# Kernel optimization log

Hardware: AMD Instinct MI355X
Metric: run time of the kernel (lower is better)

## Reference

```python
import jax, jax.numpy as jnp
import numpy as np
from jax import lax

B, C, H, W = 2, 64, 384, 384
WS = 8; NH = 4; HD = C // NH; S = WS * WS  # 64 tokens per window
EPS = 1e-5


def setup_inputs() -> dict:
    key = jax.random.key(0)
    ks = jax.random.split(key, 16)
    def n(k, shape, s=0.02):
        return jax.random.normal(k, shape, jnp.float32) * s
    return {
        "x": jax.random.normal(ks[0], (B, C, H, W), jnp.float32),
        "norm1_w": jnp.ones((C,), jnp.float32), "norm1_b": jnp.zeros((C,), jnp.float32),
        "qkv_w": n(ks[1], (3 * C, C)), "qkv_b": jnp.zeros((3 * C,), jnp.float32),
        "pos_bias": n(ks[2], (1, S, NH, NH), 0.01),  # faithful: bias over (tokens, heads, heads)
        "out_w": n(ks[3], (C, C)), "out_b": jnp.zeros((C,), jnp.float32),
        "convp_w": n(ks[4], (C, C)), "convp_b": jnp.zeros((C,), jnp.float32),
        "pw1_w": n(ks[5], (C, C, 1)), "pw1_b": jnp.zeros((C,), jnp.float32),
        "dw1_w": n(ks[6], (C, 1, 3)), "dw1_b": jnp.zeros((C,), jnp.float32),
        "tok_w": n(ks[7], (C, C)), "tok_b": jnp.zeros((C,), jnp.float32),
        "norm2_w": jnp.ones((C,), jnp.float32), "norm2_b": jnp.zeros((C,), jnp.float32),
        "leff_pw_w": n(ks[8], (C, C, 1, 1)),
        "leff_dw_w": n(ks[9], (C, 1, 3, 3)), "leff_dw_b": jnp.zeros((C,), jnp.float32),
        "fc1_w": n(ks[10], (4 * C, C)), "fc1_b": jnp.zeros((4 * C,), jnp.float32),
        "fc2_w": n(ks[11], (C, 4 * C)), "fc2_b": jnp.zeros((C,), jnp.float32),
    }


def _ln_c(x, w, b):
    # channel-wise LayerNorm (Restormer 'WithBias') on (B,C,H,W), biased variance
    mu = x.mean(axis=1, keepdims=True)
    var = ((x - mu) ** 2).mean(axis=1, keepdims=True)
    return (x - mu) / jnp.sqrt(var + EPS) * w[None, :, None, None] + b[None, :, None, None]


def _lin(x, w, b):
    return x @ w.T + b


def _win_part(x):
    # (B,C,H,W) -> (B*nw, S, C); H,W divisible by WS so pad is a no-op
    b = x.shape[0]
    x = x.reshape(b, C, H // WS, WS, W // WS, WS)
    return x.transpose(0, 2, 4, 3, 5, 1).reshape(-1, S, C)


def _win_merge(wins):
    b = wins.shape[0] // ((H // WS) * (W // WS))
    x = wins.reshape(b, H // WS, W // WS, WS, WS, C)
    return x.transpose(0, 5, 1, 3, 2, 4).reshape(b, C, H, W)


def _remsa(xw, qkv_w, qkv_b, pos_bias, out_w, out_b, convp_w, convp_b,
           pw1_w, pw1_b, dw1_w, dw1_b, tok_w, tok_b):
    bw = xw.shape[0]
    qkv = _lin(xw, qkv_w, qkv_b).reshape(bw, S, NH, 3 * HD)
    q, k, v = jnp.split(qkv, 3, axis=-1)  # each (bw, S, NH, HD)
    # Faithful to source: NO head transpose -> attention mixes across the heads axis
    scores = jnp.einsum('bshd,bsgd->bshg', q, k) * (HD ** -0.5) + pos_bias  # (bw,S,NH,NH)
    attn = jax.nn.softmax(scores, axis=-1)
    ao = jnp.einsum('bshg,bsgd->bshd', attn, v).reshape(bw, S, C)
    ao = _lin(ao, out_w, out_b)
    # convolutional branch
    xc = _lin(xw, convp_w, convp_b).transpose(0, 2, 1)  # (bw, C, S)
    xc = jnp.einsum('bcs,oc->bos', xc, pw1_w[:, :, 0]) + pw1_b[None, :, None]  # 1x1 conv1d
    xc = lax.conv_general_dilated(xc, dw1_w, (1,), 'SAME', feature_group_count=C,
                                  dimension_numbers=('NCH', 'OIH', 'NCH')) + dw1_b[None, :, None]
    xc = _lin(xc.transpose(0, 2, 1), tok_w, tok_b)
    return ao + xc


def _leff(x, pw_w, dw_w, dw_b, fc1_w, fc1_b, fc2_w, fc2_b):
    b = x.shape[0]
    y = lax.conv_general_dilated(x, pw_w, (1, 1), 'SAME',
                                 dimension_numbers=('NCHW', 'OIHW', 'NCHW'))  # 1x1, no bias
    y = lax.conv_general_dilated(y, dw_w, (1, 1), 'SAME', feature_group_count=C,
                                 dimension_numbers=('NCHW', 'OIHW', 'NCHW')) + dw_b[None, :, None, None]
    y = y.transpose(0, 2, 3, 1).reshape(b, H * W, C)
    y = jax.nn.gelu(_lin(y, fc1_w, fc1_b), approximate=False)
    y = _lin(y, fc2_w, fc2_b)
    return y.reshape(b, H, W, C).transpose(0, 3, 1, 2)


def reference(x, norm1_w, norm1_b, qkv_w, qkv_b, pos_bias, out_w, out_b,
              convp_w, convp_b, pw1_w, pw1_b, dw1_w, dw1_b, tok_w, tok_b,
              norm2_w, norm2_b, leff_pw_w, leff_dw_w, leff_dw_b,
              fc1_w, fc1_b, fc2_w, fc2_b):
    xw = _win_part(_ln_c(x, norm1_w, norm1_b))
    r = _win_merge(_remsa(xw, qkv_w, qkv_b, pos_bias, out_w, out_b, convp_w, convp_b,
                          pw1_w, pw1_b, dw1_w, dw1_b, tok_w, tok_b))
    x = x + r
    x = x + _leff(_ln_c(x, norm2_w, norm2_b), leff_pw_w, leff_dw_w, leff_dw_b,
                  fc1_w, fc1_b, fc2_w, fc2_b)
    return x
```

## Files before the change

### kernel.cpp

```cpp
#include <hip/hip_runtime.h>
#include <hip/hip_bf16.h>
#include <math.h>

#define Bn 2
#define Cc 64
#define Hh 384
#define Ww 384
#define HW (Hh*Ww)
#define Tt (Bn*HW)

using f32x4  = __attribute__((ext_vector_type(4))) float;
using bf16x8 = __attribute__((ext_vector_type(8))) short;


__device__ __forceinline__ unsigned short f2bf_u(float f) {
  return __builtin_bit_cast(unsigned short, __float2bfloat16(f));
}
__device__ __forceinline__ float bf2f(unsigned short u) {
  union { unsigned u; float f; } v; v.u = ((unsigned)u) << 16;
  return v.f;
}
__device__ __forceinline__ float gelu_exact(float v) {
  return 0.5f * v * (1.0f + erff(v * 0.70710678118654752f));
}


__global__ __launch_bounds__(512, 4) void kA(
    const float* __restrict__ x, unsigned short* __restrict__ x1g, unsigned short* __restrict__ yg,
    const float* __restrict__ n1w, const float* __restrict__ n1b,
    const float* __restrict__ qkvw, const float* __restrict__ qkvb,
    const float* __restrict__ posb,
    const float* __restrict__ outw, const float* __restrict__ outb,
    const float* __restrict__ cpw, const float* __restrict__ cpb,
    const float* __restrict__ pw1w, const float* __restrict__ pw1b,
    const float* __restrict__ dw1w, const float* __restrict__ dw1b,
    const float* __restrict__ tokw, const float* __restrict__ tokb,
    const float* __restrict__ n2w, const float* __restrict__ n2b,
    const float* __restrict__ lpw) {
  __shared__ char sX[16384];
  __shared__ char sW0[8192];
  __shared__ char sW1[8192];
  __shared__ char sQ[49152];

  const int tid = threadIdx.x;
  const int lane = tid & 63, wid = tid >> 6;
  const int fr = lane & 15, kq = lane >> 4;
  const int rtok = wid * 16 + fr;
  const int c0own = kq * 16;
  const int iy = wid, ix = fr;
  const int blk = blockIdx.x;
  const int b = blk / 1152;
  const int rr = blk - b * 1152;
  const int wy = rr / 24, wxp = rr - (rr / 24) * 24;
  const int h0 = wy * 8, w0 = wxp * 16;
  const long ibase = (long)b * HW;

  float4 wr0, wr1;
  const int wrow = tid >> 3, wc0 = (tid & 7) * 8;
  auto WLOAD = [&](const float* g) {
    const float* p = g + (long)wrow * 64 + wc0;
    wr0 = *(const float4*)p; wr1 = *(const float4*)(p + 4);
  };
  auto WSTORE = [&](char* dst) {
    bf16x8 o;
    o[0]=(short)f2bf_u(wr0.x); o[1]=(short)f2bf_u(wr0.y); o[2]=(short)f2bf_u(wr0.z); o[3]=(short)f2bf_u(wr0.w);
    o[4]=(short)f2bf_u(wr1.x); o[5]=(short)f2bf_u(wr1.y); o[6]=(short)f2bf_u(wr1.z); o[7]=(short)f2bf_u(wr1.w);
    *(bf16x8*)(dst + wrow * 128 + ((2 * wc0) ^ ((wrow & 7) << 4))) = o;
  };

  WLOAD(cpw);
  const float* xb = x + ((long)(b * 64 + c0own)) * HW + (long)(h0 + iy) * Ww + (w0 + ix);
  float vx[16]; float s0 = 0.f, s1 = 0.f;
#pragma unroll
  for (int k = 0; k < 16; ++k) {
    float v = xb[(long)k * HW];
    vx[k] = v; s0 += v; s1 += v * v;
  }
  s0 += __shfl_xor(s0, 16); s0 += __shfl_xor(s0, 32);
  s1 += __shfl_xor(s1, 16); s1 += __shfl_xor(s1, 32);
  {
    float m = s0 * (1.f / 64.f);
    float ri = rsqrtf(s1 * (1.f / 64.f) - m * m + 1e-5f);
    const int swz = (rtok & 7) << 4;
#pragma unroll
    for (int q8 = 0; q8 < 2; ++q8) {
      bf16x8 o;
#pragma unroll
      for (int j = 0; j < 8; ++j) {
        int c = c0own + q8 * 8 + j;
        o[j] = (short)f2bf_u((vx[q8 * 8 + j] - m) * ri * n1w[c] + n1b[c]);
      }
      *(bf16x8*)(sX + rtok * 128 + ((c0own * 2 + q8 * 16) ^ swz)) = o;
    }
  }
  WSTORE(sW0); WLOAD(pw1w);
  __syncthreads();

  f32x4 acc[4], res[4];
  auto ZERO = [&](f32x4 a[4]) {
#pragma unroll
    for (int nt = 0; nt < 4; ++nt) a[nt] = (f32x4){0.f, 0.f, 0.f, 0.f};
  };
  auto GEMM = [&](const char* A, const char* W, f32x4 a[4]) {
    __builtin_amdgcn_s_setprio(1);
#pragma unroll
    for (int kh = 0; kh < 2; ++kh) {
      const int arow = wid * 16 + fr;
      bf16x8 af = *(const bf16x8*)(A + arow * 128 + ((kh * 64 + kq * 16) ^ ((arow & 7) << 4)));
#pragma unroll
      for (int nt = 0; nt < 4; ++nt) {
        const int brow = nt * 16 + fr;
        bf16x8 bv = *(const bf16x8*)(W + brow * 128 + ((kh * 64 + kq * 16) ^ ((brow & 7) << 4)));
        a[nt] = __builtin_amdgcn_mfma_f32_16x16x32_bf16(af, bv, a[nt], 0, 0, 0);
      }
    }
    __builtin_amdgcn_s_setprio(0);
  };
  auto EPI = [&](char* dst, f32x4 a[4], const float* bias) {
    const int rb = wid * 16 + kq * 4;
#pragma unroll
    for (int nt = 0; nt < 4; ++nt) {
      const int col = nt * 16 + fr;
      const float bv = bias[col];
#pragma unroll
      for (int reg = 0; reg < 4; ++reg) {
        const int row = rb + reg;
        *(unsigned short*)(dst + row * 128 + ((2 * col) ^ ((row & 7) << 4))) = f2bf_u(a[nt][reg] + bv);
      }
    }
  };
  char* t0 = sQ; char* t1 = sQ + 16384; char* t2 = sQ + 32768;
  float* sQf = (float*)sQ;

  ZERO(acc); GEMM(sX, sW0, acc); EPI(t0, acc, cpb);
  WSTORE(sW1); WLOAD(tokw);
  __syncthreads();
  ZERO(acc); GEMM(t0, sW1, acc); EPI(t1, acc, pw1b);
  WSTORE(sW0); WLOAD(qkvw);
  __syncthreads();
  {
    const int c = tid & 63, tq = tid >> 6;
    const int wl = tq >> 2, chunk = tq & 3;
    float wv0 = dw1w[c * 3], wv1 = dw1w[c * 3 + 1], wv2 = dw1w[c * 3 + 2], bia = dw1b[c];
#pragma unroll
    for (int k = 0; k < 16; ++k) {
      int s = chunk * 16 + k;
      int r0 = ((s >> 3) << 4) + wl * 8 + (s & 7);
      float v = bia + bf2f(*(const unsigned short*)(t1 + r0 * 128 + ((2 * c) ^ ((r0 & 7) << 4)))) * wv1;
      if (s > 0) {
        int rm = (((s - 1) >> 3) << 4) + wl * 8 + ((s - 1) & 7);
        v += bf2f(*(const unsigned short*)(t1 + rm * 128 + ((2 * c) ^ ((rm & 7) << 4)))) * wv0;
      }
      if (s < 63) {
        int rp = (((s + 1) >> 3) << 4) + wl * 8 + ((s + 1) & 7);
        v += bf2f(*(const unsigned short*)(t1 + rp * 128 + ((2 * c) ^ ((rp & 7) << 4)))) * wv2;
      }
      *(unsigned short*)(t0 + r0 * 128 + ((2 * c) ^ ((r0 & 7) << 4))) = f2bf_u(v);
    }
  }
  WSTORE(sW1); WLOAD(qkvw + 4096);
  __syncthreads();
  ZERO(res); GEMM(t0, sW0, res);
  __syncthreads();
  ZERO(acc); GEMM(sX, sW1, acc); EPI(t0, acc, qkvb);
  WSTORE(sW0); WLOAD(qkvw + 8192);
  __syncthreads();
  ZERO(acc); GEMM(sX, sW0, acc); EPI(t1, acc, qkvb + 64);
  WSTORE(sW1); WLOAD(outw);
  __syncthreads();
  ZERO(acc); GEMM(sX, sW1, acc); EPI(t2, acc, qkvb + 128);
  WSTORE(sW0); WLOAD(lpw);
  __syncthreads();
  {
    const int r = rtok;
    const int h = kq;
    const int s = ((r >> 4) << 3) + (r & 7);
    const int swz = (r & 7) << 4;
    auto LD16 = [&](int gcol, float* o) {
      const char* base = sQ + ((gcol >> 6) * 16384) + r * 128;
      int c0 = (gcol & 63) * 2;
      bf16x8 u = *(const bf16x8*)(base + (c0 ^ swz));
      bf16x8 w2_ = *(const bf16x8*)(base + ((c0 + 16) ^ swz));
#pragma unroll
      for (int j = 0; j < 8; ++j) {
        o[j] = bf2f((unsigned short)u[j]); o[8 + j] = bf2f((unsigned short)w2_[j]);
      }
    };
    float q0[16];
    LD16(48 * h, q0);
    float sc[4];
#pragma unroll
    for (int g = 0; g < 4; ++g) {
      float kk[16]; LD16(48 * g + 16, kk);
      float a = 0.f;
#pragma unroll
      for (int d = 0; d < 16; ++d) a += q0[d] * kk[d];
      sc[g] = a * 0.25f + posb[s * 16 + h * 4 + g];
    }
    float m = fmaxf(fmaxf(sc[0], sc[1]), fmaxf(sc[2], sc[3]));
    float e[4]; float tsum = 0.f;
#pragma unroll
    for (int g = 0; g < 4; ++g) { e[g] = __expf(sc[g] - m); tsum += e[g]; }
    float inv = 1.f / tsum;
    float ao[16];
#pragma unroll
    for (int d = 0; d < 16; ++d) ao[d] = 0.f;
#pragma unroll
    for (int g = 0; g < 4; ++g) {
      float vv[16]; LD16(48 * g + 32, vv);
#pragma unroll
      for (int d = 0; d < 16; ++d) ao[d] += e[g] * vv[d];
    }
    bf16x8 o1, o2;
#pragma unroll
    for (int j = 0; j < 8; ++j) { o1[j] = (short)f2bf_u(ao[j] * inv); o2[j] = (short)f2bf_u(ao[8 + j] * inv); }
    *(bf16x8*)(sX + r * 128 + ((h * 32) ^ swz)) = o1;
    *(bf16x8*)(sX + r * 128 + ((h * 32 + 16) ^ swz)) = o2;
  }
  WSTORE(sW1);
  __syncthreads();
  GEMM(sX, sW0, res);
  {
    const int rb = wid * 16 + kq * 4;
#pragma unroll
    for (int nt = 0; nt < 4; ++nt) {
      const int col = nt * 16 + fr;
      const float ob = outb[col] + tokb[col];
#pragma unroll
      for (int reg = 0; reg < 4; ++reg)
        sQf[(rb + reg) * 67 + col] = res[nt][reg] + ob;
    }
  }
  {
    float ss0 = 0.f, ss1 = 0.f;
#pragma unroll
    for (int k = 0; k < 16; ++k) {
      float v = sQf[rtok * 67 + c0own + k] + vx[k];
      vx[k] = v; ss0 += v; ss1 += v * v;
    }
    ss0 += __shfl_xor(ss0, 16); ss0 += __shfl_xor(ss0, 32);
    ss1 += __shfl_xor(ss1, 16); ss1 += __shfl_xor(ss1, 32);
    float m = ss0 * (1.f / 64.f);
    float ri = rsqrtf(ss1 * (1.f / 64.f) - m * m + 1e-5f);
    const int swz = (rtok & 7) << 4;
    long t = ibase + (long)(h0 + iy) * Ww + (w0 + ix);
#pragma unroll
    for (int q8 = 0; q8 < 2; ++q8) {
      bf16x8 xo, no;
#pragma unroll
      for (int j = 0; j < 8; ++j) {
        int c = c0own + q8 * 8 + j;
        float v = vx[q8 * 8 + j];
        xo[j] = (short)f2bf_u(v);
        no[j] = (short)f2bf_u((v - m) * ri * n2w[c] + n2b[c]);
      }
      *(bf16x8*)((char*)x1g + t * 128 + (c0own + q8 * 8) * 2) = xo;
      *(bf16x8*)(sX + rtok * 128 + ((c0own * 2 + q8 * 16) ^ swz)) = no;
    }
  }
  ZERO(acc); GEMM(sX, sW1, acc);
  {
    const int rb = wid * 16 + kq * 4;
#pragma unroll
    for (int nt = 0; nt < 4; ++nt) {
      const int col = nt * 16 + fr;
#pragma unroll
      for (int reg = 0; reg < 4; ++reg)
        sQf[(rb + reg) * 67 + col] = acc[nt][reg];
    }
  }
  {
    long t = ibase + (long)(h0 + iy) * Ww + (w0 + ix);
#pragma unroll
    for (int q8 = 0; q8 < 2; ++q8) {
      bf16x8 o;
#pragma unroll
      for (int j = 0; j < 8; ++j)
        o[j] = (short)f2bf_u(sQf[rtok * 67 + c0own + q8 * 8 + j]);
      *(bf16x8*)((char*)yg + t * 128 + (c0own + q8 * 8) * 2) = o;
    }
  }
}


__global__ __launch_bounds__(512, 2) void kB(
    const unsigned short* __restrict__ yg, const unsigned short* __restrict__ x1g,
    float* __restrict__ out,
    const float* __restrict__ ldw, const float* __restrict__ ldb,
    const float* __restrict__ f1w, const float* __restrict__ f1b,
    const float* __restrict__ f2w, const float* __restrict__ f2b) {
  __shared__ char sZ0[8192];
  __shared__ char sZ1[8192];
  __shared__ char U[33792];
  __shared__ float wtab[640];

  const int tid = threadIdx.x;
  const int lane = tid & 63, wid = tid >> 6;
  const int fr = lane & 15, kq = lane >> 4;
  const int t_own = wid >> 2;
  const int wv = wid & 3;
  const int bid = blockIdx.x;
  const int b = bid / 1152;
  const int r2 = bid - b * 1152;
  const int hp = r2 / 6, wseg = r2 - (r2 / 6) * 6;
  const int h0 = hp * 2, w0 = wseg * 64;
  const long ibase = (long)b * HW;
  const int cbase = fr;
  const int rbase = wv * 16 + kq * 4;

  float4 wr0, wr1;
  const int wrow = tid >> 3, wc0 = (tid & 7) * 8;
  auto WLOAD = [&](const float* g, int rs) {
    const float* p = g + (long)wrow * rs + wc0;
    wr0 = *(const float4*)p; wr1 = *(const float4*)(p + 4);
  };
  auto WSTORE = [&](char* dst) {
    bf16x8 o;
    o[0]=(short)f2bf_u(wr0.x); o[1]=(short)f2bf_u(wr0.y); o[2]=(short)f2bf_u(wr0.z); o[3]=(short)f2bf_u(wr0.w);
    o[4]=(short)f2bf_u(wr1.x); o[5]=(short)f2bf_u(wr1.y); o[6]=(short)f2bf_u(wr1.z); o[7]=(short)f2bf_u(wr1.w);
    *(bf16x8*)(dst + wrow * 128 + ((2 * wc0) ^ ((wrow & 7) << 4))) = o;
  };

  unsigned short x1r[4][4];
  {
    const long p0t = ibase + (long)(h0 + t_own) * Ww + w0;
#pragma unroll
    for (int nt = 0; nt < 4; ++nt) {
      int col = nt * 16 + cbase;
#pragma unroll
      for (int reg = 0; reg < 4; ++reg)
        x1r[nt][reg] = x1g[(p0t + rbase + reg) * 64 + col];
    }
  }

#pragma unroll
  for (int it = 0; it < 2; ++it) {
    int idx = it * 512 + tid;
    if (idx < 576) wtab[idx] = ldw[(idx & 63) * 9 + (idx >> 6)];
    else if (idx < 640) wtab[idx] = ldb[idx - 576];
  }

  for (int it = 0; it < 5; ++it) {
    int idx = it * 512 + tid;
    if (idx >= 2112) break;
    int hr = idx / 528;
    int rq = idx - hr * 528;
    int px = rq >> 3, c8 = rq & 7;
    int h = h0 - 1 + hr, w = w0 - 1 + px;
    uint4 v = make_uint4(0, 0, 0, 0);
    if (h >= 0 && h < Hh && w >= 0 && w < Ww) {
      long t = ibase + (long)h * Ww + w;
      v = *(const uint4*)((const char*)yg + t * 128 + c8 * 16);
    }
    int X = hr * 66 + px;
    *(uint4*)(U + X * 128 + ((c8 * 16) ^ ((X & 7) << 4))) = v;
  }
  WLOAD(f1w, 64);
  __syncthreads();

  {
    const int c8l = tid & 7;
    const int c0 = c8l * 8;
#pragma unroll
    for (int it = 0; it < 2; ++it) {
      int task = it * 512 + tid;
      int r = task >> 9;
      int px = (task >> 3) & 63;
      float a8[8];
#pragma unroll
      for (int j = 0; j < 8; ++j) a8[j] = wtab[576 + c0 + j];
#pragma unroll
      for (int dy = 0; dy < 3; ++dy)
#pragma unroll
        for (int dx = 0; dx < 3; ++dx) {
          int X = (r + dy) * 66 + px + dx;
          bf16x8 v = *(const bf16x8*)(U + X * 128 + ((c8l * 16) ^ ((X & 7) << 4)));
          const float* wk = wtab + (dy * 3 + dx) * 64 + c0;
#pragma unroll
          for (int j = 0; j < 8; ++j) a8[j] += bf2f((unsigned short)v[j]) * wk[j];
        }
      char* sZ = r ? sZ1 : sZ0;
      bf16x8 o;
#pragma unroll
      for (int j = 0; j < 8; ++j) o[j] = (short)f2bf_u(a8[j]);
      *(bf16x8*)(sZ + px * 128 + ((c8l * 16) ^ ((px & 7) << 4))) = o;
    }
  }
  __syncthreads();

  char* sWa = U;
  char* sH0 = U + 8192;
  char* sH1 = U + 16384;
  char* sWb = U + 24576;
  char* sZt = t_own ? sZ1 : sZ0;
  char* sHt = t_own ? sH1 : sH0;
  f32x4 res[4];
#pragma unroll
  for (int nt = 0; nt < 4; ++nt) res[nt] = (f32x4){0.f, 0.f, 0.f, 0.f};

  WSTORE(sWa);
  WLOAD(f2w, 256);
  __syncthreads();

  for (int jc = 0; jc < 4; ++jc) {
    {
      f32x4 acc[4];
#pragma unroll
      for (int nt = 0; nt < 4; ++nt) acc[nt] = (f32x4){0.f, 0.f, 0.f, 0.f};
      __builtin_amdgcn_s_setprio(1);
#pragma unroll
      for (int kh = 0; kh < 2; ++kh) {
        const int arow = wv * 16 + fr;
        bf16x8 af = *(const bf16x8*)(sZt + arow * 128 + ((kh * 64 + kq * 16) ^ ((arow & 7) << 4)));
#pragma unroll
        for (int nt = 0; nt < 4; ++nt) {
          const int brow = nt * 16 + fr;
          bf16x8 bv = *(const bf16x8*)(sWa + brow * 128 + ((kh * 64 + kq * 16) ^ ((brow & 7) << 4)));
          acc[nt] = __builtin_amdgcn_mfma_f32_16x16x32_bf16(af, bv, acc[nt], 0, 0, 0);
        }
      }
      __builtin_amdgcn_s_setprio(0);
      WSTORE(sWb);
      if (jc < 3) WLOAD(f1w + (jc + 1) * 4096, 64);
#pragma unroll
      for (int nt = 0; nt < 4; ++nt) {
        const int col = nt * 16 + cbase;
        const float bv = f1b[jc * 64 + col];
#pragma unroll
        for (int reg = 0; reg < 4; ++reg) {
          const int row = rbase + reg;
          *(unsigned short*)(sHt + row * 128 + ((col * 2) ^ ((row & 7) << 4))) =
              f2bf_u(gelu_exact(acc[nt][reg] + bv));
        }
      }
    }
    __syncthreads();
    __builtin_amdgcn_s_setprio(1);
#pragma unroll
    for (int kh = 0; kh < 2; ++kh) {
      const int arow = wv * 16 + fr;
      bf16x8 af = *(const bf16x8*)(sHt + arow * 128 + ((kh * 64 + kq * 16) ^ ((arow & 7) << 4)));
#pragma unroll
      for (int nt = 0; nt < 4; ++nt) {
        const int brow = nt * 16 + fr;
        bf16x8 bv = *(const bf16x8*)(sWb + brow * 128 + ((kh * 64 + kq * 16) ^ ((brow & 7) << 4)));
        res[nt] = __builtin_amdgcn_mfma_f32_16x16x32_bf16(af, bv, res[nt], 0, 0, 0);
      }
    }
    __builtin_amdgcn_s_setprio(0);
    if (jc < 3) { WSTORE(sWa); WLOAD(f2w + (jc + 1) * 64, 256); }
    __syncthreads();
  }

  float* sO = (float*)U;
#pragma unroll
  for (int nt = 0; nt < 4; ++nt) {
    const int col = nt * 16 + cbase;
    const float bv = f2b[col];
#pragma unroll
    for (int reg = 0; reg < 4; ++reg) {
      const int row = rbase + reg;
      sO[t_own * 4160 + row * 65 + col] = res[nt][reg] + bv + bf2f(x1r[nt][reg]);
    }
  }
  __syncthreads();
  {
    const int t = tid >> 8;
    const int tt = tid & 255;
#pragma unroll
    for (int it = 0; it < 16; ++it) {
      int c = it * 4 + (tt >> 6);
      int wo = tt & 63;
      out[(((long)(b * Cc + c)) * Hh + (h0 + t)) * Ww + w0 + wo] = sO[t * 4160 + wo * 65 + c];
    }
  }
}


extern "C" void kernel_launch(void* const* d_in, const int* in_sizes, int n_in,
                              void* d_out, int out_size, void* d_ws, size_t ws_size,
                              hipStream_t stream) {
  const float* x    = (const float*)d_in[0];
  const float* n1w  = (const float*)d_in[1];
  const float* n1b  = (const float*)d_in[2];
  const float* qkvw = (const float*)d_in[3];
  const float* qkvb = (const float*)d_in[4];
  const float* posb = (const float*)d_in[5];
  const float* outw = (const float*)d_in[6];
  const float* outb = (const float*)d_in[7];
  const float* cpw  = (const float*)d_in[8];
  const float* cpb  = (const float*)d_in[9];
  const float* pw1w = (const float*)d_in[10];
  const float* pw1b = (const float*)d_in[11];
  const float* dw1w = (const float*)d_in[12];
  const float* dw1b = (const float*)d_in[13];
  const float* tokw = (const float*)d_in[14];
  const float* tokb = (const float*)d_in[15];
  const float* n2w  = (const float*)d_in[16];
  const float* n2b  = (const float*)d_in[17];
  const float* lpw  = (const float*)d_in[18];
  const float* ldw  = (const float*)d_in[19];
  const float* ldb  = (const float*)d_in[20];
  const float* f1w  = (const float*)d_in[21];
  const float* f1b  = (const float*)d_in[22];
  const float* f2w  = (const float*)d_in[23];
  const float* f2b  = (const float*)d_in[24];
  float* out = (float*)d_out;

  unsigned short* x1 = (unsigned short*)d_ws;
  unsigned short* y  = x1 + (size_t)Tt * 64;

  kA<<<dim3(2304), dim3(512), 0, stream>>>(x, x1, y, n1w, n1b, qkvw, qkvb, posb,
                                           outw, outb, cpw, cpb, pw1w, pw1b,
                                           dw1w, dw1b, tokw, tokb, n2w, n2b, lpw);
  kB<<<dim3(2304), dim3(512), 0, stream>>>(y, x1, out, ldw, ldb, f1w, f1b, f2w, f2b);
}
```

Baseline: 159.8 us.

## Pre-convert weights to bf16 once and stage them via direct global-to-LDS loads

A small prologue kernel converts all 64x64 weight tiles to bf16 once, writing them into workspace in row-major order. The main kernels then stage each tile straight into shared memory with async global_load_lds, using a swizzled source address. This replaces the per-block register load, fp32-to-bf16 conversion and LDS store. The aim is to cut per-block conversion work and register pressure and to overlap weight staging with compute. In exchange it adds a kernel launch and relies on barriers to order the async LDS writes.

```diff
diff --git a/kernel.cpp b/kernel.cpp
--- a/kernel.cpp
+++ b/kernel.cpp
@@ -12,6 +12,9 @@
 using f32x4  = __attribute__((ext_vector_type(4))) float;
 using bf16x8 = __attribute__((ext_vector_type(8))) short;
 
+typedef __attribute__((address_space(1))) const unsigned int GU;
+typedef __attribute__((address_space(3))) unsigned int LU;
+
 
 __device__ __forceinline__ unsigned short f2bf_u(float f) {
   return __builtin_bit_cast(unsigned short, __float2bfloat16(f));
@@ -25,18 +28,50 @@
 }
 
 
+__global__ __launch_bounds__(256) void kW(
+    const float* __restrict__ cpw, const float* __restrict__ pw1w,
+    const float* __restrict__ tokw, const float* __restrict__ qkvw,
+    const float* __restrict__ outw, const float* __restrict__ lpw,
+    const float* __restrict__ f1w, const float* __restrict__ f2w,
+    unsigned short* __restrict__ wt) {
+  const int tile = blockIdx.x;
+  const int tid = threadIdx.x;
+  const int row = tid >> 2, c0 = (tid & 3) * 16;
+  const float* src; int rs = 64;
+  switch (tile) {
+    case 0: src = cpw; break;
+    case 1: src = pw1w; break;
+    case 2: src = tokw; break;
+    case 3: src = qkvw; break;
+    case 4: src = qkvw + 4096; break;
+    case 5: src = qkvw + 8192; break;
+    case 6: src = outw; break;
+    case 7: src = lpw; break;
+    case 8: case 9: case 10: case 11: src = f1w + (tile - 8) * 4096; break;
+    default: src = f2w + (tile - 12) * 64; rs = 256; break;
+  }
+  const float* p = src + (long)row * rs + c0;
+  unsigned short* dst = wt + tile * 4096 + row * 64 + c0;
+#pragma unroll
+  for (int q = 0; q < 2; ++q) {
+    float4 a = *(const float4*)(p + q * 8);
+    float4 b = *(const float4*)(p + q * 8 + 4);
+    bf16x8 o;
+    o[0]=(short)f2bf_u(a.x); o[1]=(short)f2bf_u(a.y); o[2]=(short)f2bf_u(a.z); o[3]=(short)f2bf_u(a.w);
+    o[4]=(short)f2bf_u(b.x); o[5]=(short)f2bf_u(b.y); o[6]=(short)f2bf_u(b.z); o[7]=(short)f2bf_u(b.w);
+    *(bf16x8*)(dst + q * 8) = o;
+  }
+}
+
+
 __global__ __launch_bounds__(512, 4) void kA(
     const float* __restrict__ x, unsigned short* __restrict__ x1g, unsigned short* __restrict__ yg,
+    const unsigned short* __restrict__ wt,
     const float* __restrict__ n1w, const float* __restrict__ n1b,
-    const float* __restrict__ qkvw, const float* __restrict__ qkvb,
-    const float* __restrict__ posb,
-    const float* __restrict__ outw, const float* __restrict__ outb,
-    const float* __restrict__ cpw, const float* __restrict__ cpb,
-    const float* __restrict__ pw1w, const float* __restrict__ pw1b,
-    const float* __restrict__ dw1w, const float* __restrict__ dw1b,
-    const float* __restrict__ tokw, const float* __restrict__ tokb,
-    const float* __restrict__ n2w, const float* __restrict__ n2b,
-    const float* __restrict__ lpw) {
+    const float* __restrict__ qkvb, const float* __restrict__ posb,
+    const float* __restrict__ outb, const float* __restrict__ cpb,
+    const float* __restrict__ pw1b, const float* __restrict__ dw1w, const float* __restrict__ dw1b,
+    const float* __restrict__ tokb, const float* __restrict__ n2w, const float* __restrict__ n2b) {
   __shared__ char sX[16384];
   __shared__ char sW0[8192];
   __shared__ char sW1[8192];
@@ -55,20 +90,15 @@
   const int h0 = wy * 8, w0 = wxp * 16;
   const long ibase = (long)b * HW;
 
-  float4 wr0, wr1;
-  const int wrow = tid >> 3, wc0 = (tid & 7) * 8;
-  auto WLOAD = [&](const float* g) {
-    const float* p = g + (long)wrow * 64 + wc0;
-    wr0 = *(const float4*)p; wr1 = *(const float4*)(p + 4);
+  const int srow = tid >> 3;
+  const int sb = (tid & 7) * 16;
+  const int sofs = srow * 128 + (sb ^ ((srow & 7) << 4));
+  auto STAGE = [&](char* dstW, int tile) {
+    const char* src = (const char*)wt + tile * 8192 + sofs;
+    __builtin_amdgcn_global_load_lds((GU*)src, (LU*)(dstW + (tid >> 6) * 1024), 16, 0, 0);
   };
-  auto WSTORE = [&](char* dst) {
-    bf16x8 o;
-    o[0]=(short)f2bf_u(wr0.x); o[1]=(short)f2bf_u(wr0.y); o[2]=(short)f2bf_u(wr0.z); o[3]=(short)f2bf_u(wr0.w);
-    o[4]=(short)f2bf_u(wr1.x); o[5]=(short)f2bf_u(wr1.y); o[6]=(short)f2bf_u(wr1.z); o[7]=(short)f2bf_u(wr1.w);
-    *(bf16x8*)(dst + wrow * 128 + ((2 * wc0) ^ ((wrow & 7) << 4))) = o;
-  };
-
-  WLOAD(cpw);
+
+  STAGE(sW0, 0);
   const float* xb = x + ((long)(b * 64 + c0own)) * HW + (long)(h0 + iy) * Ww + (w0 + ix);
   float vx[16]; float s0 = 0.f, s1 = 0.f;
 #pragma unroll
@@ -93,7 +123,6 @@
       *(bf16x8*)(sX + rtok * 128 + ((c0own * 2 + q8 * 16) ^ swz)) = o;
     }
   }
-  WSTORE(sW0); WLOAD(pw1w);
   __syncthreads();
 
   f32x4 acc[4], res[4];
@@ -133,11 +162,12 @@
   float* sQf = (float*)sQ;
 
   ZERO(acc); GEMM(sX, sW0, acc); EPI(t0, acc, cpb);
-  WSTORE(sW1); WLOAD(tokw);
+  STAGE(sW1, 1);
   __syncthreads();
   ZERO(acc); GEMM(t0, sW1, acc); EPI(t1, acc, pw1b);
-  WSTORE(sW0); WLOAD(qkvw);
-  __syncthreads();
+  STAGE(sW0, 2);
+  __syncthreads();
+  STAGE(sW1, 3);
   {
     const int c = tid & 63, tq = tid >> 6;
     const int wl = tq >> 2, chunk = tq & 3;
@@ -158,19 +188,19 @@
       *(unsigned short*)(t0 + r0 * 128 + ((2 * c) ^ ((r0 & 7) << 4))) = f2bf_u(v);
     }
   }
-  WSTORE(sW1); WLOAD(qkvw + 4096);
   __syncthreads();
   ZERO(res); GEMM(t0, sW0, res);
   __syncthreads();
   ZERO(acc); GEMM(sX, sW1, acc); EPI(t0, acc, qkvb);
-  WSTORE(sW0); WLOAD(qkvw + 8192);
+  STAGE(sW0, 4);
   __syncthreads();
   ZERO(acc); GEMM(sX, sW0, acc); EPI(t1, acc, qkvb + 64);
-  WSTORE(sW1); WLOAD(outw);
+  STAGE(sW1, 5);
   __syncthreads();
   ZERO(acc); GEMM(sX, sW1, acc); EPI(t2, acc, qkvb + 128);
-  WSTORE(sW0); WLOAD(lpw);
-  __syncthreads();
+  STAGE(sW0, 6);
+  __syncthreads();
+  STAGE(sW1, 7);
   {
     const int r = rtok;
     const int h = kq;
@@ -217,7 +247,6 @@
     *(bf16x8*)(sX + r * 128 + ((h * 32) ^ swz)) = o1;
     *(bf16x8*)(sX + r * 128 + ((h * 32 + 16) ^ swz)) = o2;
   }
-  WSTORE(sW1);
   __syncthreads();
   GEMM(sX, sW0, res);
   {
@@ -285,10 +314,9 @@
 
 __global__ __launch_bounds__(512, 2) void kB(
     const unsigned short* __restrict__ yg, const unsigned short* __restrict__ x1g,
-    float* __restrict__ out,
+    float* __restrict__ out, const unsigned short* __restrict__ wt,
     const float* __restrict__ ldw, const float* __restrict__ ldb,
-    const float* __restrict__ f1w, const float* __restrict__ f1b,
-    const float* __restrict__ f2w, const float* __restrict__ f2b) {
+    const float* __restrict__ f1b, const float* __restrict__ f2b) {
   __shared__ char sZ0[8192];
   __shared__ char sZ1[8192];
   __shared__ char U[33792];
@@ -308,17 +336,12 @@
   const int cbase = fr;
   const int rbase = wv * 16 + kq * 4;
 
-  float4 wr0, wr1;
-  const int wrow = tid >> 3, wc0 = (tid & 7) * 8;
-  auto WLOAD = [&](const float* g, int rs) {
-    const float* p = g + (long)wrow * rs + wc0;
-    wr0 = *(const float4*)p; wr1 = *(const float4*)(p + 4);
-  };
-  auto WSTORE = [&](char* dst) {
-    bf16x8 o;
-    o[0]=(short)f2bf_u(wr0.x); o[1]=(short)f2bf_u(wr0.y); o[2]=(short)f2bf_u(wr0.z); o[3]=(short)f2bf_u(wr0.w);
-    o[4]=(short)f2bf_u(wr1.x); o[5]=(short)f2bf_u(wr1.y); o[6]=(short)f2bf_u(wr1.z); o[7]=(short)f2bf_u(wr1.w);
-    *(bf16x8*)(dst + wrow * 128 + ((2 * wc0) ^ ((wrow & 7) << 4))) = o;
+  const int srow = tid >> 3;
+  const int sb = (tid & 7) * 16;
+  const int sofs = srow * 128 + (sb ^ ((srow & 7) << 4));
+  auto STAGE = [&](char* dstW, int tile) {
+    const char* src = (const char*)wt + tile * 8192 + sofs;
+    __builtin_amdgcn_global_load_lds((GU*)src, (LU*)(dstW + (tid >> 6) * 1024), 16, 0, 0);
   };
 
   unsigned short x1r[4][4];
@@ -355,7 +378,6 @@
     int X = hr * 66 + px;
     *(uint4*)(U + X * 128 + ((c8 * 16) ^ ((X & 7) << 4))) = v;
   }
-  WLOAD(f1w, 64);
   __syncthreads();
 
   {
@@ -398,11 +420,11 @@
 #pragma unroll
   for (int nt = 0; nt < 4; ++nt) res[nt] = (f32x4){0.f, 0.f, 0.f, 0.f};
 
-  WSTORE(sWa);
-  WLOAD(f2w, 256);
+  STAGE(sWa, 8);
   __syncthreads();
 
   for (int jc = 0; jc < 4; ++jc) {
+    STAGE(sWb, 12 + jc);
     {
       f32x4 acc[4];
 #pragma unroll
@@ -420,8 +442,6 @@
         }
       }
       __builtin_amdgcn_s_setprio(0);
-      WSTORE(sWb);
-      if (jc < 3) WLOAD(f1w + (jc + 1) * 4096, 64);
 #pragma unroll
       for (int nt = 0; nt < 4; ++nt) {
         const int col = nt * 16 + cbase;
@@ -435,6 +455,7 @@
       }
     }
     __syncthreads();
+    if (jc < 3) STAGE(sWa, 9 + jc);
     __builtin_amdgcn_s_setprio(1);
 #pragma unroll
     for (int kh = 0; kh < 2; ++kh) {
@@ -448,7 +469,6 @@
       }
     }
     __builtin_amdgcn_s_setprio(0);
-    if (jc < 3) { WSTORE(sWa); WLOAD(f2w + (jc + 1) * 64, 256); }
     __syncthreads();
   }
 
@@ -509,9 +529,10 @@
 
   unsigned short* x1 = (unsigned short*)d_ws;
   unsigned short* y  = x1 + (size_t)Tt * 64;
-
-  kA<<<dim3(2304), dim3(512), 0, stream>>>(x, x1, y, n1w, n1b, qkvw, qkvb, posb,
-                                           outw, outb, cpw, cpb, pw1w, pw1b,
-                                           dw1w, dw1b, tokw, tokb, n2w, n2b, lpw);
-  kB<<<dim3(2304), dim3(512), 0, stream>>>(y, x1, out, ldw, ldb, f1w, f1b, f2w, f2b);
-}
+  unsigned short* wt = y + (size_t)Tt * 64;
+
+  kW<<<dim3(16), dim3(256), 0, stream>>>(cpw, pw1w, tokw, qkvw, outw, lpw, f1w, f2w, wt);
+  kA<<<dim3(2304), dim3(512), 0, stream>>>(x, x1, y, wt, n1w, n1b, qkvb, posb,
+                                           outb, cpb, pw1b, dw1w, dw1b, tokb, n2w, n2b);
+  kB<<<dim3(2304), dim3(512), 0, stream>>>(y, x1, out, wt, ldw, ldb, f1b, f2b);
+}
```

Result: slower. 163.4 us (+2.2%).
